# Performance work log

Measured on AMD Instinct MI355X. Metric: run time of the kernel, lower is better.

## Reference

```python
import jax, jax.numpy as jnp
import numpy as np

WH, WW = 7, 7
N_WIN_TOKENS = WH * WW
NUM_HEADS = 8
DIM = 256
HEAD_DIM = DIM // NUM_HEADS
SCALE = HEAD_DIM ** -0.5


def _relative_position_index(wh, ww):
    ch = np.arange(wh)
    cw = np.arange(ww)
    coords = np.stack(np.meshgrid(ch, cw, indexing='ij')).reshape(2, -1)  # [2, N]
    rel = coords[:, :, None] - coords[:, None, :]                         # [2, N, N]
    rel = rel.transpose(1, 2, 0).copy()                                   # [N, N, 2]
    rel[..., 0] += wh - 1
    rel[..., 1] += ww - 1
    rel[..., 0] *= 2 * ww - 1
    return jnp.asarray(rel.sum(-1))                                       # [N, N] int

REL_IDX = _relative_position_index(WH, WW)


def setup_inputs() -> dict:
    key = jax.random.key(0)
    ks = jax.random.split(key, 7)
    B_, nW = 4096, 64
    return {
        'x': jax.random.normal(ks[0], (B_, N_WIN_TOKENS, DIM), jnp.float32),
        'mask': jax.random.normal(ks[1], (nW, N_WIN_TOKENS, N_WIN_TOKENS), jnp.float32),
        'qkv_w': jax.random.normal(ks[2], (3 * DIM, DIM), jnp.float32) * 0.02,
        'qkv_b': jax.random.normal(ks[3], (3 * DIM,), jnp.float32) * 0.02,
        'proj_w': jax.random.normal(ks[4], (DIM, DIM), jnp.float32) * 0.02,
        'proj_b': jax.random.normal(ks[5], (DIM,), jnp.float32) * 0.02,
        'bias_table': jax.random.normal(ks[6], ((2 * WH - 1) * (2 * WW - 1), NUM_HEADS), jnp.float32) * 0.02,
    }


def reference(x, mask, qkv_w, qkv_b, proj_w, proj_b, bias_table):
    B_, N, C = x.shape
    H, D = NUM_HEADS, HEAD_DIM
    qkv = x @ qkv_w.T + qkv_b                           # [B_, N, 3C]
    qkv = qkv.reshape(B_, N, 3, H, D).transpose(2, 0, 3, 1, 4)
    q, k, v = qkv[0], qkv[1], qkv[2]                    # each [B_, H, N, D]
    attn = jnp.einsum('bhnd,bhmd->bhnm', q * SCALE, k)  # [B_, H, N, N]
    bias = bias_table[REL_IDX]                          # [N, N, H]
    attn = attn + bias.transpose(2, 0, 1)[None]
    nW = mask.shape[0]
    attn = attn.reshape(B_ // nW, nW, H, N, N) + mask[None, :, None]
    attn = attn.reshape(B_, H, N, N)
    attn = jax.nn.softmax(attn, axis=-1)
    out = jnp.einsum('bhnm,bhmd->bhnd', attn, v)        # [B_, H, N, D]
    out = out.transpose(0, 2, 1, 3).reshape(B_, N, C)
    out = out @ proj_w.T + proj_b
    return (out, attn)
```

## Files before the change

kernel.cpp:

```cpp
#include <hip/hip_runtime.h>
#include <hip/hip_bf16.h>

typedef __hip_bfloat16 bf16;
typedef __attribute__((ext_vector_type(8))) short bf16x8;
typedef __attribute__((ext_vector_type(4))) float f32x4;

#define NTOK   49
#define CDIM   256
#define NHEADS 8
#define HDIM   32
#define NWIN   64
#define BWIN   4096
#define MROWS  (BWIN * NTOK)
#define QKVC   768
#define SCALE  0.17677669529663687f

__device__ __forceinline__ unsigned short f2bf(float f) {
    unsigned int u = __float_as_uint(f);
    u += 0x7fffu + ((u >> 16) & 1u);
    return (unsigned short)(u >> 16);
}

__device__ __forceinline__ void load_lds16(const void* g, void* l) {
    __builtin_amdgcn_global_load_lds(
        (const __attribute__((address_space(1))) void*)g,
        (__attribute__((address_space(3))) void*)l, 16, 0, 0);
}

__global__ __launch_bounds__(256) void cvt_k(
    const float* __restrict__ x, bf16* __restrict__ xb)
{
    const long long NX = (long long)MROWS * CDIM / 4;
    const long long stride = (long long)gridDim.x * 256;
    for (long long i = (long long)blockIdx.x * 256 + threadIdx.x;
         i < NX; i += stride) {
        float4 v = ((const float4*)x)[i];
        ushort4 o;
        o.x = f2bf(v.x); o.y = f2bf(v.y); o.z = f2bf(v.z); o.w = f2bf(v.w);
        ((ushort4*)xb)[i] = o;
    }
}

__global__ __launch_bounds__(256) void qkv_gemm_mfma(
    const bf16* __restrict__ A, const float* __restrict__ W,
    const float* __restrict__ bias, bf16* __restrict__ qkv)
{
    __shared__ bf16 As[128 * 64];
    __shared__ bf16 Bs[128 * 64];
    const int tid = threadIdx.x;
    const int wid = tid >> 6;
    const int ln  = tid & 63;

    const int lin   = blockIdx.y * gridDim.x + blockIdx.x;
    const int chunk = (gridDim.x * gridDim.y) >> 3;
    const int swz   = (lin & 7) * chunk + (lin >> 3);
    const int rowBase = (swz / gridDim.x) * 128;
    const int colBase = (swz % gridDim.x) * 128;

    const int wr = wid >> 1, wc = wid & 1;

    f32x4 zero = {0.f, 0.f, 0.f, 0.f};
    f32x4 acc[4][4];
#pragma unroll
    for (int i = 0; i < 4; ++i)
#pragma unroll
        for (int j = 0; j < 4; ++j) acc[i][j] = zero;

    const int srow  = ln >> 3;
    const int gslot = ln & 7;
    const int sslotA = gslot ^ srow;
    const int swslotB = gslot ^ srow;
    const size_t aRow0 = (size_t)(rowBase + wid * 32);
    const size_t bRow0 = (size_t)(colBase + wid * 32);

    for (int k0 = 0; k0 < CDIM; k0 += 64) {
#pragma unroll
        for (int c = 0; c < 4; ++c) {
            const bf16* ga = A + (aRow0 + c * 8 + srow) * CDIM + k0 + sslotA * 8;
            load_lds16(ga, &As[(wid * 32 + c * 8) * 64]);
        }
        float4 f0[4], f1[4];
#pragma unroll
        for (int c = 0; c < 4; ++c) {
            const float* gw = W + (size_t)(bRow0 + c * 8 + srow) * CDIM
                              + k0 + gslot * 8;
            f0[c] = *(const float4*)gw;
            f1[c] = *(const float4*)(gw + 4);
        }
#pragma unroll
        for (int c = 0; c < 4; ++c) {
            bf16x8 pk;
            pk[0] = (short)f2bf(f0[c].x); pk[1] = (short)f2bf(f0[c].y);
            pk[2] = (short)f2bf(f0[c].z); pk[3] = (short)f2bf(f0[c].w);
            pk[4] = (short)f2bf(f1[c].x); pk[5] = (short)f2bf(f1[c].y);
            pk[6] = (short)f2bf(f1[c].z); pk[7] = (short)f2bf(f1[c].w);
            *(bf16x8*)((char*)Bs + (wid * 32 + c * 8 + srow) * 128
                       + (swslotB << 4)) = pk;
        }
        __syncthreads();
#pragma unroll
        for (int kk = 0; kk < 2; ++kk) {
            bf16x8 av[4], bv[4];
#pragma unroll
            for (int m = 0; m < 4; ++m) {
                int r = wr * 64 + m * 16 + (ln & 15);
                int g = kk * 4 + (ln >> 4);
                av[m] = *(const bf16x8*)((const char*)As +
                          (r * 128 + ((g ^ (r & 7)) << 4)));
            }
#pragma unroll
            for (int n = 0; n < 4; ++n) {
                int r = wc * 64 + n * 16 + (ln & 15);
                int g = kk * 4 + (ln >> 4);
                bv[n] = *(const bf16x8*)((const char*)Bs +
                          (r * 128 + ((g ^ (r & 7)) << 4)));
            }
#pragma unroll
            for (int m = 0; m < 4; ++m)
#pragma unroll
                for (int n = 0; n < 4; ++n)
                    acc[m][n] = __builtin_amdgcn_mfma_f32_16x16x32_bf16(
                        av[m], bv[n], acc[m][n], 0, 0, 0);
        }
        __syncthreads();
    }

    const int lq = ln >> 4;
    const int lr = ln & 15;
#pragma unroll
    for (int m = 0; m < 4; ++m) {
#pragma unroll
        for (int q = 0; q < 4; ++q) {
            int row = rowBase + wr * 64 + m * 16 + lq * 4 + q;
            int bw = row / NTOK;
            int nn = row - bw * NTOK;
            bf16* dst0 = qkv + (size_t)bw * 24 * (NTOK * HDIM) + nn * HDIM;
#pragma unroll
            for (int n = 0; n < 4; ++n) {
                int col = colBase + wc * 64 + n * 16 + lr;
                int which = col >> 8, hh = (col >> 5) & 7, dd = col & 31;
                float v = acc[m][n][q] + bias[col];
                dst0[(size_t)(which * 8 + hh) * (NTOK * HDIM) + dd] =
                    __float2bfloat16(v);
            }
        }
    }
}

__global__ __launch_bounds__(256) void attn_mfma_k(
    const bf16* __restrict__ qkv, const float* __restrict__ mask,
    const float* __restrict__ bt, float* __restrict__ attn_out,
    bf16* __restrict__ o_ws)
{
    const int b  = blockIdx.x;
    const int wv = threadIdx.x >> 6;
    const int ln = threadIdx.x & 63;
    const int r  = ln & 15;
    const int g  = ln >> 4;

    __shared__ short vt_all[4][32 * 64];
    __shared__ short ps_all[4][64 * 64];
    char* vt = (char*)vt_all[wv];
    char* ps = (char*)ps_all[wv];

    const float* mrow = mask + (size_t)(b & (NWIN - 1)) * (NTOK * NTOK);

#pragma unroll 1
    for (int hh = 0; hh < 2; ++hh) {
        const int h = wv + hh * 4;
        const bf16* qp = qkv + ((size_t)b * 24 + h)      * (NTOK * HDIM);
        const bf16* kp = qkv + ((size_t)b * 24 + 8 + h)  * (NTOK * HDIM);
        const bf16* vp = qkv + ((size_t)b * 24 + 16 + h) * (NTOK * HDIM);

        bf16x8 qf[4], kf[4];
#pragma unroll
        for (int t = 0; t < 4; ++t) {
            int qi = t * 16 + r; if (qi > 48) qi = 48;
            qf[t] = *(const bf16x8*)(qp + qi * HDIM + g * 8);
            kf[t] = *(const bf16x8*)(kp + qi * HDIM + g * 8);
        }

        bf16x8 vr0 = {0,0,0,0,0,0,0,0}, vr1 = vr0, vr2 = vr0, vr3 = vr0;
        if (ln < NTOK) {
            vr0 = *(const bf16x8*)(vp + ln * HDIM);
            vr1 = *(const bf16x8*)(vp + ln * HDIM + 8);
            vr2 = *(const bf16x8*)(vp + ln * HDIM + 16);
            vr3 = *(const bf16x8*)(vp + ln * HDIM + 24);
        }
#pragma unroll
        for (int d = 0; d < 32; ++d) {
            short val = (d < 8) ? vr0[d & 7] : (d < 16) ? vr1[d & 7]
                      : (d < 24) ? vr2[d & 7] : vr3[d & 7];
            *(short*)(vt + d * 128 + ((((ln >> 3)) ^ (d & 7)) << 4)
                      + (ln & 7) * 2) = val;
        }

        f32x4 zero = {0.f, 0.f, 0.f, 0.f};
        f32x4 s[4][4];
#pragma unroll
        for (int mt = 0; mt < 4; ++mt)
#pragma unroll
            for (int nt = 0; nt < 4; ++nt) s[mt][nt] = zero;
#pragma unroll
        for (int mt = 0; mt < 4; ++mt)
#pragma unroll
            for (int nt = 0; nt < 4; ++nt)
                s[mt][nt] = __builtin_amdgcn_mfma_f32_16x16x32_bf16(
                    kf[mt], qf[nt], s[mt][nt], 0, 0, 0);

        float* aout = attn_out + (((size_t)b * NHEADS + h) * NTOK) * NTOK;
#pragma unroll
        for (int nt = 0; nt < 4; ++nt) {
            const int i = nt * 16 + r;
            const bool iok = (i < NTOK);
            const int ih = (i * 9363) >> 16;
            const int iw = i - ih * 7;
            float sv[4][4];
#pragma unroll
            for (int mt = 0; mt < 4; ++mt)
#pragma unroll
                for (int q = 0; q < 4; ++q) {
                    const int j = mt * 16 + g * 4 + q;
                    float v = -1e30f;
                    if (iok && j < NTOK) {
                        const int jh = (j * 9363) >> 16;
                        const int jw = j - jh * 7;
                        float bias = bt[((ih - jh + 6) * 13 +
                                         (iw - jw + 6)) * NHEADS + h];
                        v = s[mt][nt][q] * SCALE + bias + mrow[i * NTOK + j];
                    }
                    sv[mt][q] = v;
                }
            float mx = -1e30f;
#pragma unroll
            for (int mt = 0; mt < 4; ++mt)
#pragma unroll
                for (int q = 0; q < 4; ++q) mx = fmaxf(mx, sv[mt][q]);
            mx = fmaxf(mx, __shfl_xor(mx, 16));
            mx = fmaxf(mx, __shfl_xor(mx, 32));
            float sum = 0.f;
#pragma unroll
            for (int mt = 0; mt < 4; ++mt)
#pragma unroll
                for (int q = 0; q < 4; ++q) {
                    sv[mt][q] = __expf(sv[mt][q] - mx);
                    sum += sv[mt][q];
                }
            sum += __shfl_xor(sum, 16);
            sum += __shfl_xor(sum, 32);
            const float inv = 1.0f / sum;
#pragma unroll
            for (int mt = 0; mt < 4; ++mt) {
#pragma unroll
                for (int qh = 0; qh < 2; ++qh) {
                    float p0 = sv[mt][qh * 2]     * inv;
                    float p1 = sv[mt][qh * 2 + 1] * inv;
                    const int j0 = mt * 16 + g * 4 + qh * 2;
                    if (iok) {
                        if (j0 < NTOK)     aout[(size_t)i * NTOK + j0]     = p0;
                        if (j0 + 1 < NTOK) aout[(size_t)i * NTOK + j0 + 1] = p1;
                    }
                    unsigned int pk = (unsigned int)f2bf(p0) |
                                      ((unsigned int)f2bf(p1) << 16);
                    *(unsigned int*)(ps + i * 128 +
                        (((2 * mt + (g >> 1)) ^ (r & 7)) << 4) +
                        (g & 1) * 8 + qh * 4) = pk;
                }
            }
        }

        f32x4 o[4][2];
#pragma unroll
        for (int mt = 0; mt < 4; ++mt)
#pragma unroll
            for (int nt = 0; nt < 2; ++nt) o[mt][nt] = zero;
#pragma unroll
        for (int ks = 0; ks < 2; ++ks) {
            bf16x8 pa[4], vb[2];
#pragma unroll
            for (int mt = 0; mt < 4; ++mt) {
                const int row = mt * 16 + r;
                pa[mt] = *(const bf16x8*)(ps + row * 128 +
                           (((ks * 4 + g) ^ (r & 7)) << 4));
            }
#pragma unroll
            for (int nt = 0; nt < 2; ++nt) {
                const int row = nt * 16 + r;
                vb[nt] = *(const bf16x8*)(vt + row * 128 +
                           (((ks * 4 + g) ^ (r & 7)) << 4));
            }
#pragma unroll
            for (int mt = 0; mt < 4; ++mt)
#pragma unroll
                for (int nt = 0; nt < 2; ++nt)
                    o[mt][nt] = __builtin_amdgcn_mfma_f32_16x16x32_bf16(
                        pa[mt], vb[nt], o[mt][nt], 0, 0, 0);
        }

#pragma unroll
        for (int mt = 0; mt < 4; ++mt) {
#pragma unroll
            for (int q = 0; q < 4; ++q) {
                const int i = mt * 16 + g * 4 + q;
                if (i < NTOK) {
#pragma unroll
                    for (int nt = 0; nt < 2; ++nt) {
                        const int d = nt * 16 + r;
                        o_ws[((size_t)b * NTOK + i) * CDIM + h * HDIM + d] =
                            __float2bfloat16(o[mt][nt][q]);
                    }
                }
            }
        }
    }
}

__global__ __launch_bounds__(256) void proj_gemm_mfma(
    const bf16* __restrict__ A, const float* __restrict__ W,
    const float* __restrict__ bias, float* __restrict__ out)
{
    __shared__ bf16 As[128 * 64];
    __shared__ bf16 Bs[128 * 64];
    const int tid = threadIdx.x;
    const int wid = tid >> 6;
    const int ln  = tid & 63;

    const int lin   = blockIdx.y * gridDim.x + blockIdx.x;
    const int chunk = (gridDim.x * gridDim.y) >> 3;
    const int swz   = (lin & 7) * chunk + (lin >> 3);
    const int rowBase = (swz / gridDim.x) * 128;
    const int colBase = (swz % gridDim.x) * 128;

    const int wr = wid >> 1, wc = wid & 1;

    f32x4 zero = {0.f, 0.f, 0.f, 0.f};
    f32x4 acc[4][4];
#pragma unroll
    for (int i = 0; i < 4; ++i)
#pragma unroll
        for (int j = 0; j < 4; ++j) acc[i][j] = zero;

    const int srow  = ln >> 3;
    const int gslot = ln & 7;
    const int sslotA = gslot ^ srow;
    const int swslotB = gslot ^ srow;
    const size_t aRow0 = (size_t)(rowBase + wid * 32);
    const size_t bRow0 = (size_t)(colBase + wid * 32);

    for (int k0 = 0; k0 < CDIM; k0 += 64) {
#pragma unroll
        for (int c = 0; c < 4; ++c) {
            const bf16* ga = A + (aRow0 + c * 8 + srow) * CDIM + k0 + sslotA * 8;
            load_lds16(ga, &As[(wid * 32 + c * 8) * 64]);
        }
        float4 f0[4], f1[4];
#pragma unroll
        for (int c = 0; c < 4; ++c) {
            const float* gw = W + (size_t)(bRow0 + c * 8 + srow) * CDIM
                              + k0 + gslot * 8;
            f0[c] = *(const float4*)gw;
            f1[c] = *(const float4*)(gw + 4);
        }
#pragma unroll
        for (int c = 0; c < 4; ++c) {
            bf16x8 pk;
            pk[0] = (short)f2bf(f0[c].x); pk[1] = (short)f2bf(f0[c].y);
            pk[2] = (short)f2bf(f0[c].z); pk[3] = (short)f2bf(f0[c].w);
            pk[4] = (short)f2bf(f1[c].x); pk[5] = (short)f2bf(f1[c].y);
            pk[6] = (short)f2bf(f1[c].z); pk[7] = (short)f2bf(f1[c].w);
            *(bf16x8*)((char*)Bs + (wid * 32 + c * 8 + srow) * 128
                       + (swslotB << 4)) = pk;
        }
        __syncthreads();
#pragma unroll
        for (int kk = 0; kk < 2; ++kk) {
            bf16x8 av[4], bv[4];
#pragma unroll
            for (int m = 0; m < 4; ++m) {
                int r = wr * 64 + m * 16 + (ln & 15);
                int g = kk * 4 + (ln >> 4);
                av[m] = *(const bf16x8*)((const char*)As +
                          (r * 128 + ((g ^ (r & 7)) << 4)));
            }
#pragma unroll
            for (int n = 0; n < 4; ++n) {
                int r = wc * 64 + n * 16 + (ln & 15);
                int g = kk * 4 + (ln >> 4);
                bv[n] = *(const bf16x8*)((const char*)Bs +
                          (r * 128 + ((g ^ (r & 7)) << 4)));
            }
#pragma unroll
            for (int m = 0; m < 4; ++m)
#pragma unroll
                for (int n = 0; n < 4; ++n)
                    acc[m][n] = __builtin_amdgcn_mfma_f32_16x16x32_bf16(
                        av[m], bv[n], acc[m][n], 0, 0, 0);
        }
        __syncthreads();
    }

    const int lq = ln >> 4;
    const int lr = ln & 15;
#pragma unroll
    for (int m = 0; m < 4; ++m) {
#pragma unroll
        for (int q = 0; q < 4; ++q) {
            int row = rowBase + wr * 64 + m * 16 + lq * 4 + q;
            float* orow = out + (size_t)row * CDIM;
#pragma unroll
            for (int n = 0; n < 4; ++n) {
                int col = colBase + wc * 64 + n * 16 + lr;
                orow[col] = acc[m][n][q] + bias[col];
            }
        }
    }
}

extern "C" void kernel_launch(void* const* d_in, const int* in_sizes, int n_in,
                              void* d_out, int out_size, void* d_ws, size_t ws_size,
                              hipStream_t stream)
{
    const float* x      = (const float*)d_in[0];
    const float* mask   = (const float*)d_in[1];
    const float* qkv_w  = (const float*)d_in[2];
    const float* qkv_b  = (const float*)d_in[3];
    const float* proj_w = (const float*)d_in[4];
    const float* proj_b = (const float*)d_in[5];
    const float* bt     = (const float*)d_in[6];

    float* out      = (float*)d_out;
    float* attn_out = out + (size_t)MROWS * CDIM;

    bf16* qkv_ws = (bf16*)d_ws;
    bf16* xo_ws  = qkv_ws + (size_t)MROWS * QKVC;

    cvt_k<<<2048, 256, 0, stream>>>(x, xo_ws);

    qkv_gemm_mfma<<<dim3(QKVC/128, MROWS/128), 256, 0, stream>>>(
        xo_ws, qkv_w, qkv_b, qkv_ws);

    attn_mfma_k<<<dim3(BWIN), 256, 0, stream>>>(qkv_ws, mask, bt,
                                                attn_out, xo_ws);

    proj_gemm_mfma<<<dim3(CDIM/128, MROWS/128), 256, 0, stream>>>(
        xo_ws, proj_w, proj_b, out);
}
```

Before: 1.146 ms.

## Fuse x bf16 conversion into QKV GEMM and stage mask/bias in LDS

Removes the standalone fp32-to-bf16 conversion kernel for x and instead loads fp32 x directly in the QKV GEMM, converting to bf16 while writing the A tile into swizzled LDS. This drops one kernel launch and a full write-plus-read of the bf16 copy. In exchange, each GEMM column block re-reads fp32 x, which doubles the bytes per A read, and A loads no longer use the direct global-to-LDS path. Separately, the attention kernel copies the per-window mask and the relative bias table into shared memory at block start, replacing scattered global reads in the softmax loop.

```diff
diff --git a/kernel.cpp b/kernel.cpp
--- a/kernel.cpp
+++ b/kernel.cpp
@@ -27,22 +27,8 @@
         (__attribute__((address_space(3))) void*)l, 16, 0, 0);
 }
 
-__global__ __launch_bounds__(256) void cvt_k(
-    const float* __restrict__ x, bf16* __restrict__ xb)
-{
-    const long long NX = (long long)MROWS * CDIM / 4;
-    const long long stride = (long long)gridDim.x * 256;
-    for (long long i = (long long)blockIdx.x * 256 + threadIdx.x;
-         i < NX; i += stride) {
-        float4 v = ((const float4*)x)[i];
-        ushort4 o;
-        o.x = f2bf(v.x); o.y = f2bf(v.y); o.z = f2bf(v.z); o.w = f2bf(v.w);
-        ((ushort4*)xb)[i] = o;
-    }
-}
-
 __global__ __launch_bounds__(256) void qkv_gemm_mfma(
-    const bf16* __restrict__ A, const float* __restrict__ W,
+    const float* __restrict__ X, const float* __restrict__ W,
     const float* __restrict__ bias, bf16* __restrict__ qkv)
 {
     __shared__ bf16 As[128 * 64];
@@ -68,24 +54,34 @@
 
     const int srow  = ln >> 3;
     const int gslot = ln & 7;
-    const int sslotA = gslot ^ srow;
-    const int swslotB = gslot ^ srow;
+    const int wslot = gslot ^ srow;
     const size_t aRow0 = (size_t)(rowBase + wid * 32);
     const size_t bRow0 = (size_t)(colBase + wid * 32);
 
     for (int k0 = 0; k0 < CDIM; k0 += 64) {
-#pragma unroll
-        for (int c = 0; c < 4; ++c) {
-            const bf16* ga = A + (aRow0 + c * 8 + srow) * CDIM + k0 + sslotA * 8;
-            load_lds16(ga, &As[(wid * 32 + c * 8) * 64]);
-        }
-        float4 f0[4], f1[4];
+        float4 a0[4], a1[4], f0[4], f1[4];
+#pragma unroll
+        for (int c = 0; c < 4; ++c) {
+            const float* gx = X + (aRow0 + c * 8 + srow) * CDIM + k0 + gslot * 8;
+            a0[c] = *(const float4*)gx;
+            a1[c] = *(const float4*)(gx + 4);
+        }
 #pragma unroll
         for (int c = 0; c < 4; ++c) {
             const float* gw = W + (size_t)(bRow0 + c * 8 + srow) * CDIM
                               + k0 + gslot * 8;
             f0[c] = *(const float4*)gw;
             f1[c] = *(const float4*)(gw + 4);
+        }
+#pragma unroll
+        for (int c = 0; c < 4; ++c) {
+            bf16x8 pk;
+            pk[0] = (short)f2bf(a0[c].x); pk[1] = (short)f2bf(a0[c].y);
+            pk[2] = (short)f2bf(a0[c].z); pk[3] = (short)f2bf(a0[c].w);
+            pk[4] = (short)f2bf(a1[c].x); pk[5] = (short)f2bf(a1[c].y);
+            pk[6] = (short)f2bf(a1[c].z); pk[7] = (short)f2bf(a1[c].w);
+            *(bf16x8*)((char*)As + (wid * 32 + c * 8 + srow) * 128
+                       + (wslot << 4)) = pk;
         }
 #pragma unroll
         for (int c = 0; c < 4; ++c) {
@@ -95,7 +91,7 @@
             pk[4] = (short)f2bf(f1[c].x); pk[5] = (short)f2bf(f1[c].y);
             pk[6] = (short)f2bf(f1[c].z); pk[7] = (short)f2bf(f1[c].w);
             *(bf16x8*)((char*)Bs + (wid * 32 + c * 8 + srow) * 128
-                       + (swslotB << 4)) = pk;
+                       + (wslot << 4)) = pk;
         }
         __syncthreads();
 #pragma unroll
@@ -160,10 +156,15 @@
 
     __shared__ short vt_all[4][32 * 64];
     __shared__ short ps_all[4][64 * 64];
+    __shared__ float mlds[NTOK * NTOK];
+    __shared__ float btlds[169 * NHEADS];
     char* vt = (char*)vt_all[wv];
     char* ps = (char*)ps_all[wv];
 
     const float* mrow = mask + (size_t)(b & (NWIN - 1)) * (NTOK * NTOK);
+    for (int e = threadIdx.x; e < NTOK * NTOK; e += 256) mlds[e] = mrow[e];
+    for (int e = threadIdx.x; e < 169 * NHEADS; e += 256) btlds[e] = bt[e];
+    __syncthreads();
 
 #pragma unroll 1
     for (int hh = 0; hh < 2; ++hh) {
@@ -225,9 +226,9 @@
                     if (iok && j < NTOK) {
                         const int jh = (j * 9363) >> 16;
                         const int jw = j - jh * 7;
-                        float bias = bt[((ih - jh + 6) * 13 +
-                                         (iw - jw + 6)) * NHEADS + h];
-                        v = s[mt][nt][q] * SCALE + bias + mrow[i * NTOK + j];
+                        float bias = btlds[((ih - jh + 6) * 13 +
+                                            (iw - jw + 6)) * NHEADS + h];
+                        v = s[mt][nt][q] * SCALE + bias + mlds[i * NTOK + j];
                     }
                     sv[mt][q] = v;
                 }
@@ -432,16 +433,14 @@
     float* attn_out = out + (size_t)MROWS * CDIM;
 
     bf16* qkv_ws = (bf16*)d_ws;
-    bf16* xo_ws  = qkv_ws + (size_t)MROWS * QKVC;
-
-    cvt_k<<<2048, 256, 0, stream>>>(x, xo_ws);
+    bf16* o_ws   = qkv_ws + (size_t)MROWS * QKVC;
 
     qkv_gemm_mfma<<<dim3(QKVC/128, MROWS/128), 256, 0, stream>>>(
-        xo_ws, qkv_w, qkv_b, qkv_ws);
+        x, qkv_w, qkv_b, qkv_ws);
 
     attn_mfma_k<<<dim3(BWIN), 256, 0, stream>>>(qkv_ws, mask, bt,
-                                                attn_out, xo_ws);
+                                                attn_out, o_ws);
 
     proj_gemm_mfma<<<dim3(CDIM/128, MROWS/128), 256, 0, stream>>>(
-        xo_ws, proj_w, proj_b, out);
-}
+        o_ws, proj_w, proj_b, out);
+}
```

Measured after the change: 1.129 ms. No clear change (-1.4%).
